# Kernel optimization log

Measured on AMD Instinct MI355X. Metric: run time of the kernel, lower is better.

The kernel has to match this reference:

```python
import jax, jax.numpy as jnp
import numpy as np
from itertools import combinations

B, T, D = 2, 2048, 1024
H, PD = 16, 4
DH = D // H
PAIRS = list(combinations(range(PD), 2))  # 6 pairs -> plucker_dim 6

_J6 = jnp.array([[0, 0, 0, 0, 0, 1], [0, 0, 0, 0, -1, 0], [0, 0, 0, 1, 0, 0],
                 [0, 0, 1, 0, 0, 0], [0, -1, 0, 0, 0, 0], [1, 0, 0, 0, 0, 0]],
                dtype=jnp.float32)


def exterior(p1, p2):
    # p1, p2: [B,T,H,PD] -> normalized Plucker coords [B,T,H,6]
    parts = [p1[..., i] * p2[..., j] - p1[..., j] * p2[..., i] for i, j in PAIRS]
    L = jnp.stack(parts, axis=-1)
    n = jnp.maximum(jnp.linalg.norm(L, axis=-1, keepdims=True), 1e-12)
    return L / n


def setup_inputs() -> dict:
    key = jax.random.key(0)
    ks = jax.random.split(key, 16)
    s = 0.02
    inp = {
        'x': jax.random.normal(ks[0], (B, T, D), jnp.float32),
        'qkv_w': jax.random.normal(ks[1], (D, 3 * D), jnp.float32) * s,
        'qkv_b': jnp.zeros((3 * D,), jnp.float32),
        'w1_write': jax.random.normal(ks[2], (D, PD * H), jnp.float32) * s,
        'w2_write': jax.random.normal(ks[3], (D, PD * H), jnp.float32) * s,
        'w1_read': jax.random.normal(ks[4], (D, PD * H), jnp.float32) * s,
        'w2_read': jax.random.normal(ks[5], (D, PD * H), jnp.float32) * s,
        'memv_w': jax.random.normal(ks[6], (D, D), jnp.float32) * s,
        'memv_b': jnp.zeros((D,), jnp.float32),
        'memg_w': jax.random.normal(ks[7], (D, H), jnp.float32) * s,
        'memg_b': jnp.zeros((H,), jnp.float32),
        'mem_scale': jnp.full((H,), 0.1, jnp.float32),
        'out_w': jax.random.normal(ks[8], (D, D), jnp.float32) * s,
        'out_b': jnp.zeros((D,), jnp.float32),
        'J': _J6,
        'decays': jnp.array([0.95] * (H // 2) + [0.999] * (H - H // 2), jnp.float32),
    }
    return inp


def reference(x, qkv_w, qkv_b, w1_write, w2_write, w1_read, w2_read,
              memv_w, memv_b, memg_w, memg_b, mem_scale, out_w, out_b, J, decays):
    Bx, Tx, Dx = x.shape
    scale = DH ** -0.5

    # --- standard causal attention branch ---
    qkv = (x @ qkv_w + qkv_b).reshape(Bx, Tx, 3, H, DH)
    q, k, v = qkv[:, :, 0], qkv[:, :, 1], qkv[:, :, 2]  # [B,T,H,dh]
    scores = jnp.einsum('bihd,bjhd->bhij', q, k) * scale
    i = jnp.arange(Tx)
    causal = i[:, None] >= i[None, :]  # keep j <= i
    scores = jnp.where(causal[None, None], scores, -jnp.inf)
    attn = jax.nn.softmax(scores, axis=-1)
    seq_out = jnp.einsum('bhij,bjhd->bihd', attn, v).reshape(Bx, Tx, Dx)

    # --- Plucker memory branch ---
    x_prev = jnp.concatenate([jnp.zeros((Bx, 1, Dx), x.dtype), x[:, :-1]], axis=1)
    w1 = (x_prev @ w1_write).reshape(Bx, Tx, H, PD)
    w2 = (x @ w2_write).reshape(Bx, Tx, H, PD)
    write_lines = exterior(w1, w2)          # [B,T,H,6]
    r1 = (x @ w1_read).reshape(Bx, Tx, H, PD)
    r2 = (x @ w2_read).reshape(Bx, Tx, H, PD)
    read_lines = exterior(r1, r2)           # [B,T,H,6]

    Jw = jnp.einsum('bthi,ij->bthj', write_lines, J)
    incidence = jnp.einsum('bihp,bjhp->bhij', read_lines, Jw)  # [B,H,T,T]
    inc_sq = incidence ** 2

    diffs = i[:, None] - i[None, :]                      # [T,T]
    lower = diffs > 0                                    # strictly past (j < i)
    dsafe = jnp.where(lower, diffs, 0).astype(x.dtype)
    weights = jnp.where(lower[None], decays[:, None, None] ** dsafe[None], 0.0)  # [H,T,T]
    mem_score = jnp.sum(inc_sq * weights[None], axis=-1)  # [B,H,T]

    mem_val = x @ memv_w + memv_b                         # [B,T,D]
    gate = jax.nn.sigmoid(x @ memg_w + memg_b)            # [B,T,H]
    gated = jax.nn.sigmoid(mem_score.transpose(0, 2, 1) * mem_scale[None, None]) * gate
    gated = jnp.mean(gated, axis=-1, keepdims=True)       # [B,T,1]

    return (seq_out + gated * mem_val) @ out_w + out_b
```

## Files before the change

kernel.cpp:

```cpp
#include <hip/hip_runtime.h>

#define BT 4096
#define Dd 1024
#define Tt 2048

typedef __attribute__((ext_vector_type(8))) short bf16x8;
typedef __attribute__((ext_vector_type(4))) float f32x4;
typedef __attribute__((ext_vector_type(4))) unsigned u32x4;

__device__ __forceinline__ short f2bf(float f) {
  unsigned u = __builtin_bit_cast(unsigned, f);
  u = (u + 0x7FFFu + ((u >> 16) & 1u)) >> 16;
  return (short)u;
}
__device__ __forceinline__ float bf2f(short s) {
  unsigned u = ((unsigned)(unsigned short)s) << 16;
  return __builtin_bit_cast(float, u);
}
__device__ __forceinline__ unsigned cvt_pk_bf16(float a, float b) {
  unsigned r;
  asm("v_cvt_pk_bf16_f32 %0, %1, %2" : "=v"(r) : "v"(a), "v"(b));
  return r;
}

__device__ __forceinline__ void load_lds16(const void* gsrc, void* ldst) {
  __builtin_amdgcn_global_load_lds(
      (const __attribute__((address_space(1))) void*)gsrc,
      (__attribute__((address_space(3))) void*)ldst, 16, 0, 0);
}

__global__ __launch_bounds__(256) void k_cvt(const float* __restrict__ src,
                                             short* __restrict__ dst, int n4) {
  int i = blockIdx.x * 256 + threadIdx.x;
  if (i >= n4) return;
  float4 v = ((const float4*)src)[i];
  short4 o;
  o.x = f2bf(v.x); o.y = f2bf(v.y); o.z = f2bf(v.z); o.w = f2bf(v.w);
  ((short4*)dst)[i] = o;
}

__global__ __launch_bounds__(256) void k_wtall(
    const float* __restrict__ qkv_w, const float* __restrict__ memv_w,
    const float* __restrict__ out_w, const float* __restrict__ w1w,
    const float* __restrict__ w2w, const float* __restrict__ w1r,
    const float* __restrict__ w2r, const float* __restrict__ memg_w,
    short* __restrict__ WTall, short* __restrict__ WTout) {
  __shared__ float tile[64][65];
  const int bid = blockIdx.x;
  const float* src;
  short* dst;
  int N, n0, k0, rowoff;
  if (bid < 768) {
    src = qkv_w; dst = WTall; N = 3072;
    n0 = (bid % 48) * 64; k0 = (bid / 48) * 64; rowoff = 0;
  } else if (bid < 1024) {
    int r = bid - 768;
    src = memv_w; dst = WTall; N = 1024;
    n0 = (r % 16) * 64; k0 = (r / 16) * 64; rowoff = 3072;
  } else if (bid < 1280) {
    int r = bid - 1024;
    src = out_w; dst = WTout; N = 1024;
    n0 = (r % 16) * 64; k0 = (r / 16) * 64; rowoff = 0;
  } else {
    int r = bid - 1280;
    int z = r / 16;
    src = z == 0 ? w1w : z == 1 ? w2w : z == 2 ? w1r : z == 3 ? w2r : memg_w;
    dst = WTall; N = (z == 4) ? 16 : 64;
    n0 = 0; k0 = (r % 16) * 64; rowoff = 4096 + z * 64;
  }
  const int c = threadIdx.x & 63, r4 = threadIdx.x >> 6;
#pragma unroll
  for (int i = 0; i < 16; ++i) {
    int r = i * 4 + r4;
    float v = 0.f;
    if (n0 + c < N) v = src[(size_t)(k0 + r) * N + n0 + c];
    tile[r][c] = v;
  }
  __syncthreads();
#pragma unroll
  for (int i = 0; i < 16; ++i) {
    int n = i * 4 + r4;
    if (n0 + n < N)
      dst[(size_t)(rowoff + n0 + n) * 1024 + k0 + c] = f2bf(tile[c][n]);
  }
}

__global__ __launch_bounds__(256, 4) void k_g128(
    const short* __restrict__ A, const short* __restrict__ Bt,
    const float* __restrict__ bias, const float* __restrict__ bias2,
    short* __restrict__ oq, short* __restrict__ ok_, short* __restrict__ ov,
    short* __restrict__ omv, float* __restrict__ ocs, int K) {
  __shared__ __align__(16) short lds[16384];
  const int tid = threadIdx.x;
  const int wid = tid >> 6, lane = tid & 63;
  const int wr = wid >> 1, wc = wid & 1;
  const int ql = lane & 15, g = lane >> 4;
  int wg = blockIdx.x, xcd = wg & 7, idx = wg >> 3;
  const int n_t = idx >> 2;
  const int m_t = xcd * 4 + (idx & 3);
  const int nkt = K >> 5;
  const int bm = m_t * 128, bn = n_t * 128;
  f32x4 acc[4][4] = {};

  const short* srcA[2];
  const short* srcB[2];
  short* dstA[2];
  short* dstB[2];
#pragma unroll
  for (int j = 0; j < 2; ++j) {
    int o16 = j * 256 + tid;
    int rr = o16 >> 2, u = o16 & 3;
    int sp = u ^ ((rr >> 1) & 3);
    srcA[j] = A + (size_t)(bm + rr) * K + sp * 8;
    srcB[j] = Bt + (size_t)(bn + rr) * K + sp * 8;
    dstA[j] = lds + o16 * 8;
    dstB[j] = lds + 8192 + o16 * 8;
  }
#define STG(D, KT)                                                            \
  do {                                                                        \
    const int k0s = (KT) << 5;                                                \
    _Pragma("unroll") for (int j = 0; j < 2; ++j) {                           \
      load_lds16(srcA[j] + k0s, dstA[j] + (D)*4096);                          \
      load_lds16(srcB[j] + k0s, dstB[j] + (D)*4096);                          \
    }                                                                         \
  } while (0)

  const int sw = (g ^ ((ql >> 1) & 3)) << 4;
  const char* bA = (const char*)lds + wr * 4096 + ql * 64 + sw;
  const char* bB = (const char*)lds + 16384 + wc * 4096 + ql * 64 + sw;

#define RD_A(DST, DOFF, MQ)                                                    \
  _Pragma("unroll") for (int mi = 0; mi < 2; ++mi)                             \
      DST[mi] = *(const bf16x8*)(bA + (DOFF) + (MQ)*2048 + mi * 1024);
#define RD_B(DST, DOFF, NQ)                                                    \
  _Pragma("unroll") for (int ni = 0; ni < 2; ++ni)                             \
      DST[ni] = *(const bf16x8*)(bB + (DOFF) + (NQ)*2048 + ni * 1024);
#define MFMA4(AF, BF, MQ, NQ)                                                  \
  _Pragma("unroll") for (int mi = 0; mi < 2; ++mi)                             \
      _Pragma("unroll") for (int ni = 0; ni < 2; ++ni)                         \
          acc[(MQ)*2 + mi][(NQ)*2 + ni] =                                      \
      __builtin_amdgcn_mfma_f32_16x16x32_bf16(                                 \
          BF[ni], AF[mi], acc[(MQ)*2 + mi][(NQ)*2 + ni], 0, 0, 0)

  STG(0, 0);

  for (int kt = 0; kt < nkt; ++kt) {
    const int d = kt & 1;
    const int dOff = d << 13;
    const bool s1 = kt + 1 < nkt;
    if (s1) {
      STG(d ^ 1, kt + 1);
      asm volatile("s_waitcnt vmcnt(4)" ::: "memory");
    } else {
      asm volatile("s_waitcnt vmcnt(0)" ::: "memory");
    }
    __builtin_amdgcn_sched_barrier(0);
    __builtin_amdgcn_s_barrier();
    bf16x8 a0[2], a1[2], b0[2], b1[2];
    RD_A(a0, dOff, 0);
    RD_A(a1, dOff, 1);
    RD_B(b0, dOff, 0);
    RD_B(b1, dOff, 1);
    asm volatile("s_waitcnt lgkmcnt(0)" ::: "memory");
    __builtin_amdgcn_sched_barrier(0);
    __builtin_amdgcn_s_setprio(1);
    MFMA4(a0, b0, 0, 0);
    MFMA4(a0, b1, 0, 1);
    MFMA4(a1, b1, 1, 1);
    MFMA4(a1, b0, 1, 0);
    __builtin_amdgcn_s_setprio(0);
    __builtin_amdgcn_sched_barrier(0);
    __builtin_amdgcn_s_barrier();
    __builtin_amdgcn_sched_barrier(0);
  }
#undef MFMA4
#undef RD_A
#undef RD_B
#undef STG

#pragma unroll
  for (int a = 0; a < 4; ++a) {
    const int m = bm + wr * 64 + a * 16 + ql;
    const int b = m >> 11, t = m & 2047;
#pragma unroll
    for (int c = 0; c < 4; ++c) {
      const int n0 = bn + wc * 64 + c * 16 + g * 4;
      f32x4 v = acc[a][c];
      if (n0 < 3072) {
        const float4 b4 = *(const float4*)&bias[n0];
        v[0] += b4.x; v[1] += b4.y; v[2] += b4.z; v[3] += b4.w;
        uint2 pk = make_uint2(cvt_pk_bf16(v[0], v[1]), cvt_pk_bf16(v[2], v[3]));
        const int sel = n0 >> 10, rem = n0 & 1023;
        if (sel == 0)
          *(uint2*)&oq[((size_t)(b * 16 + (rem >> 6)) * 2048 + t) * 64 + (rem & 63)] = pk;
        else if (sel == 1)
          *(uint2*)&ok_[((size_t)(b * 16 + (rem >> 6)) * 2048 + t) * 64 + (rem & 63)] = pk;
        else
          *(uint2*)&ov[(size_t)(b * 2048 + t) * 1024 + rem] = pk;
      } else if (n0 < 4096) {
        const float4 b4 = *(const float4*)&bias2[n0 - 3072];
        v[0] += b4.x; v[1] += b4.y; v[2] += b4.z; v[3] += b4.w;
        uint2 pk = make_uint2(cvt_pk_bf16(v[0], v[1]), cvt_pk_bf16(v[2], v[3]));
        *(uint2*)&omv[(size_t)(b * 2048 + t) * 1024 + n0 - 3072] = pk;
      } else if (n0 < 4368) {
        *(f32x4*)&ocs[(size_t)(b * 2048 + t) * 272 + n0 - 4096] = v;
      }
    }
  }
}

__global__ __launch_bounds__(256, 4) void k_gout(
    const short* __restrict__ A, const short* __restrict__ Bt,
    const float* __restrict__ bias, float* __restrict__ C, int K) {
  __shared__ __align__(16) short lds[8192];
  const int tid = threadIdx.x;
  const int wid = tid >> 6, lane = tid & 63;
  const int wr = wid >> 1, wc = wid & 1;
  const int ql = lane & 15, g = lane >> 4;
  int wg = blockIdx.x, xcd = wg & 7, idx = wg >> 3;
  const int n_t = idx >> 3, m_t = xcd * 8 + (idx & 7);
  const int bm = m_t * 64, bn = n_t * 64;
  const int nkt = K >> 5;
  f32x4 acc[2][2] = {};

  const short* srcA;
  const short* srcB;
  short* dstA;
  short* dstB;
  {
    int rr = tid >> 2, u = tid & 3;
    int sp = u ^ ((rr >> 1) & 3);
    srcA = A + (size_t)(bm + rr) * K + sp * 8;
    srcB = Bt + (size_t)(bn + rr) * K + sp * 8;
    dstA = lds + tid * 8;
    dstB = lds + 4096 + tid * 8;
  }
#define STG(D, KT)                                                            \
  do {                                                                        \
    const int k0s = (KT) << 5;                                                \
    load_lds16(srcA + k0s, dstA + (D)*2048);                                  \
    load_lds16(srcB + k0s, dstB + (D)*2048);                                  \
  } while (0)

  const int sw = (g ^ ((ql >> 1) & 3)) << 4;
  const char* bA = (const char*)lds + wr * 2048 + ql * 64 + sw;
  const char* bB = (const char*)lds + 8192 + wc * 2048 + ql * 64 + sw;

  STG(0, 0);

  for (int kt = 0; kt < nkt; ++kt) {
    const int d = kt & 1;
    const int dOff = d << 12;
    const bool s1 = kt + 1 < nkt;
    if (s1) {
      STG(d ^ 1, kt + 1);
      asm volatile("s_waitcnt vmcnt(2)" ::: "memory");
    } else {
      asm volatile("s_waitcnt vmcnt(0)" ::: "memory");
    }
    __builtin_amdgcn_sched_barrier(0);
    __builtin_amdgcn_s_barrier();
    bf16x8 af[2], bf2[2];
#pragma unroll
    for (int mi = 0; mi < 2; ++mi)
      af[mi] = *(const bf16x8*)(bA + dOff + mi * 1024);
#pragma unroll
    for (int ni = 0; ni < 2; ++ni)
      bf2[ni] = *(const bf16x8*)(bB + dOff + ni * 1024);
    asm volatile("s_waitcnt lgkmcnt(0)" ::: "memory");
    __builtin_amdgcn_sched_barrier(0);
    __builtin_amdgcn_s_setprio(1);
#pragma unroll
    for (int mi = 0; mi < 2; ++mi)
#pragma unroll
      for (int ni = 0; ni < 2; ++ni)
        acc[mi][ni] = __builtin_amdgcn_mfma_f32_16x16x32_bf16(
            bf2[ni], af[mi], acc[mi][ni], 0, 0, 0);
    __builtin_amdgcn_s_setprio(0);
    __builtin_amdgcn_sched_barrier(0);
    __builtin_amdgcn_s_barrier();
    __builtin_amdgcn_sched_barrier(0);
  }
#undef STG

#pragma unroll
  for (int a = 0; a < 2; ++a) {
    const int m = bm + wr * 32 + a * 16 + ql;
#pragma unroll
    for (int c = 0; c < 2; ++c) {
      const int n0 = bn + wc * 32 + c * 16 + g * 4;
      f32x4 v = acc[a][c];
      const float4 b4 = *(const float4*)&bias[n0];
      v[0] += b4.x; v[1] += b4.y; v[2] += b4.z; v[3] += b4.w;
      *(f32x4*)&C[(size_t)m * 1024 + n0] = v;
    }
  }
}

__global__ __launch_bounds__(256) void k_vtrans(const short* __restrict__ vtmp,
                                                short* __restrict__ vb) {
  __shared__ short tile[64][68];
  const int bh = blockIdx.x, b = bh >> 4, h = bh & 15;
  const int t0 = blockIdx.y * 64;
  const int tid = threadIdx.x;
#pragma unroll
  for (int pass = 0; pass < 16; ++pass) {
    int r = pass * 4 + (tid >> 6);
    int c = tid & 63;
    tile[r][c] = vtmp[((size_t)(b * 2048) + t0 + r) * 1024 + h * 64 + c];
  }
  __syncthreads();
#pragma unroll
  for (int pass = 0; pass < 16; ++pass) {
    int r = pass * 4 + (tid >> 6);
    int c = tid & 63;
    int cp = (c & 32) | (((c >> 2) & 3) << 3) | (((c >> 4) & 1) << 2) | (c & 3);
    vb[(((size_t)b * 16 + h) * 64 + r) * 2048 + t0 + cp] = tile[c][r];
  }
}

#define ATT_SCALE 0.18033688f

__device__ __forceinline__ void attn_core(const bf16x8 qa[2], f32x4 o[4],
                                          float& m, float& l,
                                          const short* __restrict__ Kc,
                                          const short* __restrict__ Vc,
                                          int qt, int kt, int qglob,
                                          int ql, int g) {
  const int kv0 = kt * 64;
  f32x4 s4[4];
  __builtin_amdgcn_s_setprio(1);
#pragma unroll
  for (int nt = 0; nt < 4; ++nt) {
    int krow = nt * 16 + ql;
    f32x4 s = {0.f, 0.f, 0.f, 0.f};
#pragma unroll
    for (int kc = 0; kc < 2; ++kc) {
      int sl = (kc * 4 + g) ^ (krow & 7);
      bf16x8 af = *(const bf16x8*)&Kc[krow * 64 + sl * 8];
      s = __builtin_amdgcn_mfma_f32_16x16x32_bf16(af, qa[kc], s, 0, 0, 0);
    }
    s4[nt] = s;
  }
  __builtin_amdgcn_s_setprio(0);
  float mt = -1e30f;
  const bool diag = (kt == qt);
#pragma unroll
  for (int nt = 0; nt < 4; ++nt)
#pragma unroll
    for (int rg = 0; rg < 4; ++rg) {
      float v = s4[nt][rg] * ATT_SCALE;
      if (diag) {
        int kk = kv0 + nt * 16 + g * 4 + rg;
        v = (kk <= qglob) ? v : -1e30f;
      }
      s4[nt][rg] = v;
      mt = fmaxf(mt, v);
    }
  mt = fmaxf(mt, __shfl_xor(mt, 16, 64));
  mt = fmaxf(mt, __shfl_xor(mt, 32, 64));
  float mnew = fmaxf(m, mt);
  float sf = __builtin_amdgcn_exp2f(m - mnew);
  m = mnew;
  float rs = 0.f;
#pragma unroll
  for (int nt = 0; nt < 4; ++nt)
#pragma unroll
    for (int rg = 0; rg < 4; ++rg) {
      float p = __builtin_amdgcn_exp2f(s4[nt][rg] - mnew);
      s4[nt][rg] = p;
      rs += p;
    }
  rs += __shfl_xor(rs, 16, 64);
  rs += __shfl_xor(rs, 32, 64);
  l = l * sf + rs;
#pragma unroll
  for (int nt = 0; nt < 4; ++nt) o[nt] *= sf;
  bf16x8 pf[2];
#pragma unroll
  for (int kc = 0; kc < 2; ++kc) {
    u32x4 w;
    w[0] = cvt_pk_bf16(s4[2 * kc][0], s4[2 * kc][1]);
    w[1] = cvt_pk_bf16(s4[2 * kc][2], s4[2 * kc][3]);
    w[2] = cvt_pk_bf16(s4[2 * kc + 1][0], s4[2 * kc + 1][1]);
    w[3] = cvt_pk_bf16(s4[2 * kc + 1][2], s4[2 * kc + 1][3]);
    pf[kc] = __builtin_bit_cast(bf16x8, w);
  }
  __builtin_amdgcn_s_setprio(1);
#pragma unroll
  for (int nt2 = 0; nt2 < 4; ++nt2) {
    int d = nt2 * 16 + ql;
#pragma unroll
    for (int kc = 0; kc < 2; ++kc) {
      int sl = (kc * 4 + g) ^ (d & 7);
      bf16x8 vf = *(const bf16x8*)&Vc[d * 64 + sl * 8];
      o[nt2] = __builtin_amdgcn_mfma_f32_16x16x32_bf16(vf, pf[kc], o[nt2], 0, 0, 0);
    }
  }
  __builtin_amdgcn_s_setprio(0);
}

__device__ __forceinline__ void attn_epi(const f32x4 o[4], float l,
                                         short* __restrict__ Fb,
                                         const short* __restrict__ mvb,
                                         const float* __restrict__ gm,
                                         float* ep,
                                         int b, int h, int qt, int wave, int lane) {
  const int ql = lane & 15, g = lane >> 4;
  float inv = 1.f / l;
#pragma unroll
  for (int nt2 = 0; nt2 < 4; ++nt2) {
    f32x4 v = o[nt2] * inv;
    *(f32x4*)&ep[ql * 64 + (((nt2 * 4 + g) ^ (ql & 7)) << 2)] = v;
  }
  const size_t rowbase = ((size_t)b * 2048 + qt * 64 + wave * 16);
  short* srow = Fb + rowbase * 1024 + h * 64;
  const short* mrow = mvb + rowbase * 1024 + h * 64;
  const float* grow = gm + rowbase;
#pragma unroll
  for (int p = 0; p < 8; ++p) {
    int prow = p * 2 + (lane >> 5);
    int d2 = (lane & 31) * 2;
    const float* rp = &ep[prow * 64 + (((d2 >> 2) ^ (prow & 7)) << 2) + (d2 & 3)];
    float2 vv = *(const float2*)rp;
    float gg = grow[prow];
    unsigned mvp = *(const unsigned*)&mrow[(size_t)prow * 1024 + d2];
    float m0 = bf2f((short)(mvp & 0xffff));
    float m1 = bf2f((short)(mvp >> 16));
    *(unsigned*)&srow[(size_t)prow * 1024 + d2] =
        cvt_pk_bf16(vv.x + gg * m0, vv.y + gg * m1);
  }
}

__global__ __launch_bounds__(256, 2) void k_attn(const short* __restrict__ Q,
                                                 const short* __restrict__ Kg,
                                                 const short* __restrict__ Vg,
                                                 const short* __restrict__ mvb,
                                                 const float* __restrict__ gm,
                                                 short* __restrict__ Fb) {
  __shared__ short Kt[2][64 * 64];
  __shared__ short Vt[2][64 * 64];
  const int wg = blockIdx.x;
  const int x = wg & 7, s = wg >> 3;
  const int bh = 4 * x + (s >> 4);
  const int pi = s & 15;
  const int qtA = pi, qtB = 31 - pi;
  const int b = bh >> 4, h = bh & 15;
  const int tid = threadIdx.x;
  const int wave = tid >> 6, lane = tid & 63;
  const int ql = lane & 15, g = lane >> 4;
  const short* qbase = Q + (size_t)bh * 2048 * 64;
  const int qgA = qtA * 64 + wave * 16 + ql;
  const int qgB = qtB * 64 + wave * 16 + ql;
  bf16x8 qaA[2], qaB[2];
  {
    const short* qr = qbase + (size_t)qgA * 64;
    qaA[0] = *(const bf16x8*)&qr[g * 8];
    qaA[1] = *(const bf16x8*)&qr[32 + g * 8];
    qr = qbase + (size_t)qgB * 64;
    qaB[0] = *(const bf16x8*)&qr[g * 8];
    qaB[1] = *(const bf16x8*)&qr[32 + g * 8];
  }
  f32x4 oA[4] = {}, oB[4] = {};
  float mA = -1e30f, lA = 0.f, mB = -1e30f, lB = 0.f;
  const short* kgb = Kg + (size_t)bh * 2048 * 64;
  const short* vgb = Vg + (size_t)bh * 64 * 2048;

  auto stage = [&](int buf, int kt) {
    int kv0 = kt * 64;
#pragma unroll
    for (int j = 0; j < 2; ++j) {
      int slot = (wave * 2 + j) * 64 + lane;
      int r = slot >> 3, s8 = slot & 7;
      int ss = s8 ^ (r & 7);
      load_lds16(kgb + (size_t)(kv0 + r) * 64 + ss * 8, &Kt[buf][slot * 8]);
      load_lds16(vgb + (size_t)r * 2048 + kv0 + ss * 8, &Vt[buf][slot * 8]);
    }
  };

  stage(0, 0);
  int cur = 0;
  for (int it = 0; it < 33; ++it) {
    __syncthreads();
    if (it < 32) {
      int nit = it + 1;
      int nkt2 = (nit <= qtB) ? nit : nit - qtB - 1;
      stage(cur ^ 1, nkt2);
    }
    const short* Kc = Kt[cur];
    const short* Vc = Vt[cur];
    if (it <= qtB)
      attn_core(qaB, oB, mB, lB, Kc, Vc, qtB, it, qgB, ql, g);
    else
      attn_core(qaA, oA, mA, lA, Kc, Vc, qtA, it - qtB - 1, qgA, ql, g);
    cur ^= 1;
  }
  __syncthreads();
  float* ep = (float*)&Kt[0][0] + wave * 1024;
  attn_epi(oB, lB, Fb, mvb, gm, ep, b, h, qtB, wave, lane);
  attn_epi(oA, lA, Fb, mvb, gm, ep, b, h, qtA, wave, lane);
}

__global__ __launch_bounds__(256) void k_lines(const float* __restrict__ Cs,
                                               const float* __restrict__ Jm,
                                               float* __restrict__ u,
                                               float* __restrict__ rr) {
  int idx = blockIdx.x * 256 + threadIdx.x;
  if (idx >= 2 * 2048 * 16) return;
  int h = idx & 15, t = (idx >> 4) & 2047, b = idx >> 15;
  const float* rowx = Cs + (size_t)(b * 2048 + t) * 272;
  float w1[4], w2[4], r1[4], r2[4];
  if (t == 0) {
#pragma unroll
    for (int i = 0; i < 4; ++i) w1[i] = 0.f;
  } else {
    const float* prev = Cs + (size_t)(b * 2048 + t - 1) * 272;
#pragma unroll
    for (int i = 0; i < 4; ++i) w1[i] = prev[h * 4 + i];
  }
#pragma unroll
  for (int i = 0; i < 4; ++i) {
    w2[i] = rowx[64 + h * 4 + i];
    r1[i] = rowx[128 + h * 4 + i];
    r2[i] = rowx[192 + h * 4 + i];
  }
  const int pi[6] = {0, 0, 0, 1, 1, 2}, pj[6] = {1, 2, 3, 2, 3, 3};
  float wl[6], rl[6], nw = 0.f, nr = 0.f;
#pragma unroll
  for (int e = 0; e < 6; ++e) {
    wl[e] = w1[pi[e]] * w2[pj[e]] - w1[pj[e]] * w2[pi[e]];
    rl[e] = r1[pi[e]] * r2[pj[e]] - r1[pj[e]] * r2[pi[e]];
    nw += wl[e] * wl[e];
    nr += rl[e] * rl[e];
  }
  nw = 1.f / fmaxf(sqrtf(nw), 1e-12f);
  nr = 1.f / fmaxf(sqrtf(nr), 1e-12f);
  size_t base = (((size_t)b * 16 + h) * 2048 + t) * 6;
#pragma unroll
  for (int jc = 0; jc < 6; ++jc) {
    float s = 0.f;
#pragma unroll
    for (int i = 0; i < 6; ++i) s += wl[i] * Jm[i * 6 + jc];
    u[base + jc] = s * nw;
    rr[base + jc] = rl[jc] * nr;
  }
}

__global__ __launch_bounds__(256) void k_scanw(const float* __restrict__ u,
                                               float* __restrict__ w,
                                               const float* __restrict__ decays) {
  __shared__ float wtot[4];
  const int ch = blockIdx.x;
  const int bh = blockIdx.y;
  const float d = decays[bh & 15];
  const int p = ch / 6, q = ch % 6;
  const int tid = threadIdx.x, lane = tid & 63, wv = tid >> 6;
  const float* ub = u + (size_t)bh * 2048 * 6;
  const int t0 = tid * 8;
  float z[8];
  float a = 0.f;
#pragma unroll
  for (int i = 0; i < 8; ++i) {
    float up = ub[(t0 + i) * 6 + p], uq = ub[(t0 + i) * 6 + q];
    z[i] = up * uq;
    a = d * (a + z[i]);
  }
  float d8 = d * d; d8 *= d8; d8 *= d8;
  float I = a;
  float ds = d8;
#pragma unroll
  for (int s = 1; s < 64; s <<= 1) {
    float v = __shfl_up(I, s, 64);
    if (lane >= s) I += ds * v;
    ds *= ds;
  }
  if (lane == 63) wtot[wv] = I;
  __syncthreads();
  float carry = 0.f;
  for (int w2 = 0; w2 < wv; ++w2) carry = carry * ds + wtot[w2];
  float dlp1 = exp2f(log2f(d8) * (float)(lane + 1));
  float Ig = I + dlp1 * carry;
  float E = __shfl_up(Ig, 1, 64);
  if (lane == 0) E = carry;
  float S = E;
  float out[8];
#pragma unroll
  for (int i = 0; i < 8; ++i) {
    out[i] = S;
    S = d * (S + z[i]);
  }
  float4* wp = (float4*)(w + ((size_t)bh * 36 + ch) * 2048 + t0);
  wp[0] = make_float4(out[0], out[1], out[2], out[3]);
  wp[1] = make_float4(out[4], out[5], out[6], out[7]);
}

__global__ __launch_bounds__(256) void k_scandot(const float* __restrict__ rr,
                                                 const float* __restrict__ w,
                                                 float* __restrict__ scores) {
  const int bh = blockIdx.y;
  const int t = blockIdx.x * 256 + threadIdx.x;
  const float* rb = rr + ((size_t)bh * 2048 + t) * 6;
  float r[6];
#pragma unroll
  for (int i = 0; i < 6; ++i) r[i] = rb[i];
  const float* wb = w + (size_t)bh * 36 * 2048 + t;
  float acc = 0.f;
#pragma unroll
  for (int ch = 0; ch < 36; ++ch)
    acc += r[ch / 6] * r[ch % 6] * wb[(size_t)ch * 2048];
  scores[(size_t)bh * 2048 + t] = acc;
}

__global__ __launch_bounds__(256) void k_gate(const float* __restrict__ scores,
                                              const float* __restrict__ Cs,
                                              const float* __restrict__ memg_b,
                                              const float* __restrict__ mem_scale,
                                              float* __restrict__ gmean) {
  int idx = blockIdx.x * 256 + threadIdx.x;
  if (idx >= BT) return;
  int b = idx >> 11, t = idx & 2047;
  float acc = 0.f;
#pragma unroll
  for (int h = 0; h < 16; ++h) {
    float s = scores[((size_t)(b * 16 + h) * 2048) + t];
    float gl = Cs[(size_t)idx * 272 + 256 + h] + memg_b[h];
    float a = 1.f / (1.f + __expf(-s * mem_scale[h]));
    float gg = 1.f / (1.f + __expf(-gl));
    acc += a * gg;
  }
  gmean[idx] = acc * (1.f / 16.f);
}

extern "C" void kernel_launch(void* const* d_in, const int* in_sizes, int n_in,
                              void* d_out, int out_size, void* d_ws, size_t ws_size,
                              hipStream_t stream) {
  const float* x = (const float*)d_in[0];
  const float* qkv_w = (const float*)d_in[1];
  const float* qkv_b = (const float*)d_in[2];
  const float* w1w = (const float*)d_in[3];
  const float* w2w = (const float*)d_in[4];
  const float* w1r = (const float*)d_in[5];
  const float* w2r = (const float*)d_in[6];
  const float* memv_w = (const float*)d_in[7];
  const float* memv_b = (const float*)d_in[8];
  const float* memg_w = (const float*)d_in[9];
  const float* memg_b = (const float*)d_in[10];
  const float* mem_scale = (const float*)d_in[11];
  const float* out_w = (const float*)d_in[12];
  const float* out_b = (const float*)d_in[13];
  const float* Jm = (const float*)d_in[14];
  const float* decays = (const float*)d_in[15];

  char* w = (char*)d_ws;
  size_t off = 0;
  auto alloc = [&](size_t bytes) -> void* {
    void* p = w + off;
    off += (bytes + 255) & ~(size_t)255;
    return p;
  };
  short* xb = (short*)alloc((size_t)BT * Dd * 2);
  short* WTall = (short*)alloc((size_t)4480 * 1024 * 2);
  short* WTout = (short*)alloc((size_t)1024 * 1024 * 2);
  short* qb = (short*)alloc((size_t)32 * 2048 * 64 * 2);
  short* kb = (short*)alloc((size_t)32 * 2048 * 64 * 2);
  short* vtmp = (short*)alloc((size_t)BT * 1024 * 2);
  short* vb = (short*)alloc((size_t)32 * 64 * 2048 * 2);
  float* Csm = (float*)alloc((size_t)BT * 272 * 4);
  float* ua = (float*)alloc((size_t)32 * 2048 * 6 * 4);
  float* ra = (float*)alloc((size_t)32 * 2048 * 6 * 4);
  float* sc = (float*)alloc((size_t)32 * 2048 * 4);
  float* gm = (float*)alloc((size_t)BT * 4);
  short* mvb = (short*)alloc((size_t)BT * 1024 * 2);
  short* Fb = (short*)alloc((size_t)BT * Dd * 2);
  float* wscan = (float*)alloc((size_t)32 * 36 * 2048 * 4);
  (void)ws_size; (void)in_sizes; (void)n_in; (void)out_size;

  k_cvt<<<(BT * Dd / 4 + 255) / 256, 256, 0, stream>>>(x, xb, BT * Dd / 4);
  k_wtall<<<1360, 256, 0, stream>>>(qkv_w, memv_w, out_w, w1w, w2w, w1r, w2r,
                                    memg_w, WTall, WTout);

  k_g128<<<1120, 256, 0, stream>>>(xb, WTall, qkv_b, memv_b,
                                   qb, kb, vtmp, mvb, Csm, 1024);

  k_lines<<<(2 * 2048 * 16 + 255) / 256, 256, 0, stream>>>(Csm, Jm, ua, ra);
  k_scanw<<<dim3(36, 32), 256, 0, stream>>>(ua, wscan, decays);
  k_scandot<<<dim3(8, 32), 256, 0, stream>>>(ra, wscan, sc);
  k_gate<<<(BT + 255) / 256, 256, 0, stream>>>(sc, Csm, memg_b, mem_scale, gm);

  k_vtrans<<<dim3(32, 32), 256, 0, stream>>>(vtmp, vb);

  k_attn<<<512, 256, 0, stream>>>(qb, kb, vb, mvb, gm, Fb);

  k_gout<<<1024, 256, 0, stream>>>(Fb, WTout, out_b, (float*)d_out, 1024);
}
```

Baseline: 165.3 us.

## Split paired causal attention tiles into separate blocks and fuse x conversion

The attention kernel previously had each block process two complementary query tiles (qt and 31-qt) sequentially for balanced work. Now each block handles a single query tile, doubling the grid to 1024 blocks and raising launch bounds to 4 blocks per CU, with tile order interleaved to spread long and short tiles across the grid. This exposes more parallelism and occupancy but gives up the per-block load balance and may raise register pressure. Separately, the x fp32-to-bf16 conversion kernel is merged into the weight-transpose launch as extra blocks, saving one kernel launch.

```diff
diff --git a/kernel.cpp b/kernel.cpp
--- a/kernel.cpp
+++ b/kernel.cpp
@@ -27,16 +27,6 @@
   __builtin_amdgcn_global_load_lds(
       (const __attribute__((address_space(1))) void*)gsrc,
       (__attribute__((address_space(3))) void*)ldst, 16, 0, 0);
-}
-
-__global__ __launch_bounds__(256) void k_cvt(const float* __restrict__ src,
-                                             short* __restrict__ dst, int n4) {
-  int i = blockIdx.x * 256 + threadIdx.x;
-  if (i >= n4) return;
-  float4 v = ((const float4*)src)[i];
-  short4 o;
-  o.x = f2bf(v.x); o.y = f2bf(v.y); o.z = f2bf(v.z); o.w = f2bf(v.w);
-  ((short4*)dst)[i] = o;
 }
 
 __global__ __launch_bounds__(256) void k_wtall(
@@ -44,9 +34,18 @@
     const float* __restrict__ out_w, const float* __restrict__ w1w,
     const float* __restrict__ w2w, const float* __restrict__ w1r,
     const float* __restrict__ w2r, const float* __restrict__ memg_w,
-    short* __restrict__ WTall, short* __restrict__ WTout) {
+    short* __restrict__ WTall, short* __restrict__ WTout,
+    const float* __restrict__ x, short* __restrict__ xb) {
   __shared__ float tile[64][65];
   const int bid = blockIdx.x;
+  if (bid >= 1360) {
+    int i = (bid - 1360) * 256 + threadIdx.x;
+    float4 v = ((const float4*)x)[i];
+    short4 o;
+    o.x = f2bf(v.x); o.y = f2bf(v.y); o.z = f2bf(v.z); o.w = f2bf(v.w);
+    ((short4*)xb)[i] = o;
+    return;
+  }
   const float* src;
   short* dst;
   int N, n0, k0, rowoff;
@@ -432,7 +431,7 @@
   }
 }
 
-__global__ __launch_bounds__(256, 2) void k_attn(const short* __restrict__ Q,
+__global__ __launch_bounds__(256, 4) void k_attn(const short* __restrict__ Q,
                                                  const short* __restrict__ Kg,
                                                  const short* __restrict__ Vg,
                                                  const short* __restrict__ mvb,
@@ -441,64 +440,48 @@
   __shared__ short Kt[2][64 * 64];
   __shared__ short Vt[2][64 * 64];
   const int wg = blockIdx.x;
-  const int x = wg & 7, s = wg >> 3;
-  const int bh = 4 * x + (s >> 4);
-  const int pi = s & 15;
-  const int qtA = pi, qtB = 31 - pi;
+  const int x = wg & 7, r = wg >> 3;
+  const int q = r >> 2, j = r & 3;
+  const int bh = 4 * x + j;
+  const int q2 = (q + 16) & 31;
+  const int qt = (j == 0) ? q : (j == 1) ? 31 - q : (j == 2) ? q2 : 31 - q2;
   const int b = bh >> 4, h = bh & 15;
   const int tid = threadIdx.x;
   const int wave = tid >> 6, lane = tid & 63;
   const int ql = lane & 15, g = lane >> 4;
-  const short* qbase = Q + (size_t)bh * 2048 * 64;
-  const int qgA = qtA * 64 + wave * 16 + ql;
-  const int qgB = qtB * 64 + wave * 16 + ql;
-  bf16x8 qaA[2], qaB[2];
-  {
-    const short* qr = qbase + (size_t)qgA * 64;
-    qaA[0] = *(const bf16x8*)&qr[g * 8];
-    qaA[1] = *(const bf16x8*)&qr[32 + g * 8];
-    qr = qbase + (size_t)qgB * 64;
-    qaB[0] = *(const bf16x8*)&qr[g * 8];
-    qaB[1] = *(const bf16x8*)&qr[32 + g * 8];
-  }
-  f32x4 oA[4] = {}, oB[4] = {};
-  float mA = -1e30f, lA = 0.f, mB = -1e30f, lB = 0.f;
+  const int qglob = qt * 64 + wave * 16 + ql;
+  const short* qr = Q + ((size_t)bh * 2048 + qglob) * 64;
+  bf16x8 qa[2];
+  qa[0] = *(const bf16x8*)&qr[g * 8];
+  qa[1] = *(const bf16x8*)&qr[32 + g * 8];
+  f32x4 o[4] = {};
+  float m = -1e30f, l = 0.f;
   const short* kgb = Kg + (size_t)bh * 2048 * 64;
   const short* vgb = Vg + (size_t)bh * 64 * 2048;
 
   auto stage = [&](int buf, int kt) {
     int kv0 = kt * 64;
 #pragma unroll
-    for (int j = 0; j < 2; ++j) {
-      int slot = (wave * 2 + j) * 64 + lane;
-      int r = slot >> 3, s8 = slot & 7;
-      int ss = s8 ^ (r & 7);
-      load_lds16(kgb + (size_t)(kv0 + r) * 64 + ss * 8, &Kt[buf][slot * 8]);
-      load_lds16(vgb + (size_t)r * 2048 + kv0 + ss * 8, &Vt[buf][slot * 8]);
+    for (int jj = 0; jj < 2; ++jj) {
+      int slot = (wave * 2 + jj) * 64 + lane;
+      int rr = slot >> 3, s8 = slot & 7;
+      int ss = s8 ^ (rr & 7);
+      load_lds16(kgb + (size_t)(kv0 + rr) * 64 + ss * 8, &Kt[buf][slot * 8]);
+      load_lds16(vgb + (size_t)rr * 2048 + kv0 + ss * 8, &Vt[buf][slot * 8]);
     }
   };
 
   stage(0, 0);
   int cur = 0;
-  for (int it = 0; it < 33; ++it) {
+  for (int it = 0; it <= qt; ++it) {
     __syncthreads();
-    if (it < 32) {
-      int nit = it + 1;
-      int nkt2 = (nit <= qtB) ? nit : nit - qtB - 1;
-      stage(cur ^ 1, nkt2);
-    }
-    const short* Kc = Kt[cur];
-    const short* Vc = Vt[cur];
-    if (it <= qtB)
-      attn_core(qaB, oB, mB, lB, Kc, Vc, qtB, it, qgB, ql, g);
-    else
-      attn_core(qaA, oA, mA, lA, Kc, Vc, qtA, it - qtB - 1, qgA, ql, g);
+    if (it < qt) stage(cur ^ 1, it + 1);
+    attn_core(qa, o, m, l, Kt[cur], Vt[cur], qt, it, qglob, ql, g);
     cur ^= 1;
   }
   __syncthreads();
   float* ep = (float*)&Kt[0][0] + wave * 1024;
-  attn_epi(oB, lB, Fb, mvb, gm, ep, b, h, qtB, wave, lane);
-  attn_epi(oA, lA, Fb, mvb, gm, ep, b, h, qtA, wave, lane);
+  attn_epi(o, l, Fb, mvb, gm, ep, b, h, qt, wave, lane);
 }
 
 __global__ __launch_bounds__(256) void k_lines(const float* __restrict__ Cs,
@@ -675,9 +658,8 @@
   float* wscan = (float*)alloc((size_t)32 * 36 * 2048 * 4);
   (void)ws_size; (void)in_sizes; (void)n_in; (void)out_size;
 
-  k_cvt<<<(BT * Dd / 4 + 255) / 256, 256, 0, stream>>>(x, xb, BT * Dd / 4);
-  k_wtall<<<1360, 256, 0, stream>>>(qkv_w, memv_w, out_w, w1w, w2w, w1r, w2r,
-                                    memg_w, WTall, WTout);
+  k_wtall<<<5456, 256, 0, stream>>>(qkv_w, memv_w, out_w, w1w, w2w, w1r, w2r,
+                                    memg_w, WTall, WTout, x, xb);
 
   k_g128<<<1120, 256, 0, stream>>>(xb, WTall, qkv_b, memv_b,
                                    qb, kb, vtmp, mvb, Csm, 1024);
@@ -689,7 +671,7 @@
 
   k_vtrans<<<dim3(32, 32), 256, 0, stream>>>(vtmp, vb);
 
-  k_attn<<<512, 256, 0, stream>>>(qb, kb, vb, mvb, gm, Fb);
+  k_attn<<<1024, 256, 0, stream>>>(qb, kb, vb, mvb, gm, Fb);
 
   k_gout<<<1024, 256, 0, stream>>>(Fb, WTout, out_b, (float*)d_out, 1024);
 }
```

Result: faster. 155.4 us (-6.0%).
